# Performance work log

Measured on AMD Instinct MI355X. Metric: run time of the kernel, lower is better.

The kernel has to match this reference:

```python
import jax, jax.numpy as jnp
import numpy as np

N_NODES = 100000
N_EDGES = 1600000
IN_DIM = 128
OUT_DIM = 64


def setup_inputs() -> dict:
    key = jax.random.key(0)
    k1, k2, k3, k4, k5, k6 = jax.random.split(key, 6)
    x = jax.random.normal(k1, (N_NODES, IN_DIM), dtype=jnp.float32)
    edge_row = jax.random.randint(k2, (N_EDGES,), 0, N_NODES, dtype=jnp.int32)
    edge_col = jax.random.randint(k3, (N_EDGES,), 0, N_NODES, dtype=jnp.int32)
    edge_val = jax.random.uniform(k4, (N_EDGES,), dtype=jnp.float32)
    W = jax.random.normal(k5, (IN_DIM, OUT_DIM), dtype=jnp.float32) * (1.0 / np.sqrt(IN_DIM))
    b = jax.random.normal(k6, (OUT_DIM,), dtype=jnp.float32) * 0.01
    return {"x": x, "edge_row": edge_row, "edge_col": edge_col,
            "edge_val": edge_val, "W": W, "b": b}


def reference(x, edge_row, edge_col, edge_val, W, b):
    # xw = Linear(x)  -> [N, OUT_DIM]
    xw = x @ W + b
    # SpMM: (A_hat @ xw)[r] = sum_e val[e] * xw[col[e]] for edges with row[e]==r
    msgs = edge_val[:, None] * xw[edge_col]          # [E, OUT_DIM]
    ax = jax.ops.segment_sum(msgs, edge_row, num_segments=N_NODES)  # [N, OUT_DIM]
    # ReLU; dropout p=0.0 is identity (eval mode)
    return jax.nn.relu(ax)
```

## Files before the change

### kernel.cpp

```cpp
#include <hip/hip_runtime.h>
#include <hip/hip_fp16.h>
#include <limits.h>

#define IN_DIM 128
#define OUT_DIM 64
#define NBUCK 782
#define RPB 128
#define HRPB 64
#define CHUNK 4096
#define SCAP2 2048


typedef _Float16 half8_t __attribute__((ext_vector_type(8)));
typedef float    f32x4  __attribute__((ext_vector_type(4)));

__device__ __forceinline__ int kmap(int g, int j) {
    return g * 4 + (j & 3) + 16 * (j >> 2);
}

__global__ __launch_bounds__(256) void prep_kernel(
    const float* __restrict__ W, __half* __restrict__ wf,
    int* __restrict__ bcount, int* __restrict__ cursor) {
    const int t = threadIdx.x;
    for (int idx = t; idx < 4 * 4 * 64 * 8; idx += 256) {
        const int j    = idx & 7;
        const int lane = (idx >> 3) & 63;
        const int ks   = (idx >> 9) & 3;
        const int n    = idx >> 11;
        const int col  = n * 16 + (lane & 15);
        const int k    = ks * 32 + kmap(lane >> 4, j);
        wf[idx] = __float2half(W[k * OUT_DIM + col]);
    }
    if (bcount)
        for (int i = t; i < NBUCK; i += 256) { bcount[i] = 0; cursor[i] = 0; }
}

__global__ __launch_bounds__(256) void gemm_hist_kernel(
    const float* __restrict__ x, const __half* __restrict__ wf,
    const float* __restrict__ b, __half* __restrict__ xw, int n_nodes,
    const int* __restrict__ erow, int* __restrict__ bcount, int n_edges) {
    __shared__ int h[NBUCK];
    const int t  = threadIdx.x;
    const int l  = t & 63;
    const int wv = t >> 6;
    const int g  = l >> 4;
    const int rowbase = blockIdx.x * 64 + wv * 16;
    const int row = rowbase + (l & 15);
    const bool rok = row < n_nodes;
    const float* xr = x + (size_t)row * IN_DIM;

    half8_t bf[4][4];
    const half8_t* wf8 = (const half8_t*)wf;
    #pragma unroll
    for (int n = 0; n < 4; ++n)
        #pragma unroll
        for (int ks = 0; ks < 4; ++ks)
            bf[n][ks] = wf8[(n * 4 + ks) * 64 + l];

    half8_t af[4];
    #pragma unroll
    for (int ks = 0; ks < 4; ++ks) {
        float4 c0 = rok ? *(const float4*)(xr + ks * 32 + g * 4)
                        : make_float4(0.f, 0.f, 0.f, 0.f);
        float4 c1 = rok ? *(const float4*)(xr + ks * 32 + 16 + g * 4)
                        : make_float4(0.f, 0.f, 0.f, 0.f);
        half8_t a;
        a[0] = (_Float16)c0.x; a[1] = (_Float16)c0.y;
        a[2] = (_Float16)c0.z; a[3] = (_Float16)c0.w;
        a[4] = (_Float16)c1.x; a[5] = (_Float16)c1.y;
        a[6] = (_Float16)c1.z; a[7] = (_Float16)c1.w;
        af[ks] = a;
    }

    f32x4 acc[4];
    #pragma unroll
    for (int n = 0; n < 4; ++n) acc[n] = (f32x4){0.f, 0.f, 0.f, 0.f};

    #pragma unroll
    for (int ks = 0; ks < 4; ++ks)
        #pragma unroll
        for (int n = 0; n < 4; ++n)
            acc[n] = __builtin_amdgcn_mfma_f32_16x16x32_f16(af[ks], bf[n][ks], acc[n], 0, 0, 0);

    float bias[4];
    #pragma unroll
    for (int n = 0; n < 4; ++n) bias[n] = b[n * 16 + (l & 15)];

    #pragma unroll
    for (int n = 0; n < 4; ++n)
        #pragma unroll
        for (int q = 0; q < 4; ++q) {
            const int ro = rowbase + g * 4 + q;
            if (ro < n_nodes)
                xw[(size_t)ro * OUT_DIM + n * 16 + (l & 15)] =
                    __float2half(acc[n][q] + bias[n]);
        }

    if (bcount && blockIdx.x < 512) {
        for (int i = t; i < NBUCK; i += 256) h[i] = 0;
        __syncthreads();
        const int stride = 512 * 256;
        for (int e = blockIdx.x * 256 + t; e < n_edges; e += stride)
            atomicAdd(&h[erow[e] >> 7], 1);
        __syncthreads();
        for (int i = t; i < NBUCK; i += 256)
            if (h[i]) atomicAdd(&bcount[i], h[i]);
    }
}

__global__ __launch_bounds__(512) void partition_kernel(
    const int* __restrict__ erow, const int* __restrict__ ecol,
    const float* __restrict__ eval_, const int* __restrict__ bcount,
    int* __restrict__ cursor, int2* __restrict__ ecs,
    int* __restrict__ bbase, int n_edges) {
    __shared__ int  hist[NBUCK];
    __shared__ int  lbase[NBUCK];
    __shared__ int  gdelta[NBUCK];
    __shared__ int  sbase[NBUCK];
    __shared__ int2 data[CHUNK];
    __shared__ int  gpos[CHUNK];
    __shared__ int  wsum[8];

    const int t = threadIdx.x;
    const int base = blockIdx.x * CHUNK;
    const int cnt = min(CHUNK, n_edges - base);

    for (int i = t; i < NBUCK; i += 512) hist[i] = 0;

    {
        const int i0 = 2 * t, i1 = 2 * t + 1;
        const int v0 = (i0 < NBUCK) ? bcount[i0] : 0;
        const int v1 = (i1 < NBUCK) ? bcount[i1] : 0;
        const int s2 = v0 + v1;
        int inc = s2;
        #pragma unroll
        for (int d = 1; d < 64; d <<= 1) {
            int u = __shfl_up(inc, d, 64);
            if ((t & 63) >= d) inc += u;
        }
        if ((t & 63) == 63) wsum[t >> 6] = inc;
        __syncthreads();
        int wp = 0;
        #pragma unroll
        for (int w = 0; w < 8; ++w) if (w < (t >> 6)) wp += wsum[w];
        const int ex = wp + (inc - s2);
        if (i0 < NBUCK) sbase[i0] = ex;
        if (i1 < NBUCK) sbase[i1] = ex + v0;
    }
    __syncthreads();

    if (blockIdx.x == 0) {
        for (int i = t; i < NBUCK; i += 512) bbase[i] = sbase[i];
        if (t == 0) bbase[NBUCK] = n_edges;
    }

    int   myrow[CHUNK / 512];
    int   mycol[CHUNK / 512];
    float myval[CHUNK / 512];
    #pragma unroll
    for (int i = 0; i < CHUNK / 512; ++i) {
        const int idx = t + i * 512;
        if (idx < cnt) {
            const int e = base + idx;
            myrow[i] = erow[e];
            mycol[i] = ecol[e];
            myval[i] = eval_[e];
            atomicAdd(&hist[myrow[i] >> 7], 1);
        }
    }
    __syncthreads();

    {
        const int i0 = 2 * t, i1 = 2 * t + 1;
        const int v0 = (i0 < NBUCK) ? hist[i0] : 0;
        const int v1 = (i1 < NBUCK) ? hist[i1] : 0;
        const int s2 = v0 + v1;
        int inc = s2;
        #pragma unroll
        for (int d = 1; d < 64; d <<= 1) {
            int u = __shfl_up(inc, d, 64);
            if ((t & 63) >= d) inc += u;
        }
        if ((t & 63) == 63) wsum[t >> 6] = inc;
        __syncthreads();
        int wp = 0;
        #pragma unroll
        for (int w = 0; w < 8; ++w) if (w < (t >> 6)) wp += wsum[w];
        const int ex = wp + (inc - s2);
        if (i0 < NBUCK) lbase[i0] = ex;
        if (i1 < NBUCK) lbase[i1] = ex + v0;
    }
    __syncthreads();

    for (int i = t; i < NBUCK; i += 512) {
        const int c = hist[i];
        gdelta[i] = c ? (sbase[i] + atomicAdd(&cursor[i], c) - lbase[i]) : 0;
    }
    __syncthreads();

    #pragma unroll
    for (int i = 0; i < CHUNK / 512; ++i) {
        const int idx = t + i * 512;
        if (idx < cnt) {
            const int bk = myrow[i] >> 7;
            const int slot = atomicAdd(&lbase[bk], 1);
            int2 p;
            p.x = (int)(((unsigned)(myrow[i] & (RPB - 1)) << 25) |
                        ((unsigned)mycol[i] << 7));
            p.y = __float_as_int(myval[i]);
            data[slot] = p;
            gpos[slot] = slot + gdelta[bk];
        }
    }
    __syncthreads();

    for (int slot = t; slot < cnt; slot += 512)
        ecs[gpos[slot]] = data[slot];
}

__global__ __launch_bounds__(512) void bucket_gather_kernel(
    const __half* __restrict__ xw, const int2* __restrict__ ecs,
    const int* __restrict__ bbase, float* __restrict__ out,
    int n_nodes, int n_edges) {
    __shared__ int2 data[SCAP2];
    __shared__ int  hist[HRPB];
    __shared__ int  rstart[HRPB + 1];

    const int bk2  = blockIdx.x;
    const int bk   = bk2 >> 1;
    const int half = bk2 & 1;
    const int t    = threadIdx.x;
    const int lane = t & 63;
    const int wv   = t >> 6;
    const int q    = lane & 7;
    const int g    = lane >> 3;

    const int s   = bbase[bk];
    const int e   = bbase[bk + 1];
    const int cnt = e - s;
    const int rowbase = bk * RPB + half * HRPB;
    const char* xwb = (const char*)xw;

    if (t < HRPB) hist[t] = 0;
    __syncthreads();

    for (int i = t; i < cnt; i += 512) {
        const unsigned rl = ((unsigned)ecs[s + i].x) >> 25;
        if ((int)(rl >> 6) == half) atomicAdd(&hist[rl & (HRPB - 1)], 1);
    }
    __syncthreads();

    if (t < HRPB) {
        const int v = hist[t];
        int inc = v;
        #pragma unroll
        for (int d = 1; d < 64; d <<= 1) {
            int u = __shfl_up(inc, d, 64);
            if (t >= d) inc += u;
        }
        rstart[t] = inc - v;
        hist[t]   = inc - v;
        if (t == HRPB - 1) rstart[HRPB] = inc;
    }
    __syncthreads();

    const int cntH = rstart[HRPB];

    if (cntH <= SCAP2) {
        for (int i = t; i < cnt; i += 512) {
            const int2 p = ecs[s + i];
            const unsigned rl = ((unsigned)p.x) >> 25;
            if ((int)(rl >> 6) == half) {
                const int pos = atomicAdd(&hist[rl & (HRPB - 1)], 1);
                data[pos] = p;
            }
        }
        __syncthreads();

        for (int rp = 0; rp < 4; ++rp) {
            const int rl0 = wv * 8 + rp * 2;
            const int rl1 = rl0 + 1;
            int j0 = rstart[rl0];
            const int e0 = rstart[rl0 + 1];
            int j1 = rstart[rl1];
            const int e1 = rstart[rl1 + 1];

            float acc0[8], acc1[8];
            #pragma unroll
            for (int i = 0; i < 8; ++i) { acc0[i] = 0.f; acc1[i] = 0.f; }

            while (j0 < e0 || j1 < e1) {
                const bool a0 = j0 < e0;
                const bool a1 = j1 < e1;
                float v0 = 0.f, v1 = 0.f;
                unsigned off0 = 0, off1 = 0;
                if (a0) {
                    const int ei = j0 + g;
                    const int2 p = data[min(ei, cntH - 1)];
                    v0 = (ei < e0) ? __int_as_float(p.y) : 0.f;
                    off0 = (((unsigned)p.x) & 0x01FFFF80u) | ((unsigned)q << 4);
                }
                if (a1) {
                    const int ei = j1 + g;
                    const int2 p = data[min(ei, cntH - 1)];
                    v1 = (ei < e1) ? __int_as_float(p.y) : 0.f;
                    off1 = (((unsigned)p.x) & 0x01FFFF80u) | ((unsigned)q << 4);
                }
                union { uint4 u; __half2 h[4]; } U0, U1;
                if (a0) U0.u = *(const uint4*)(xwb + off0);
                if (a1) U1.u = *(const uint4*)(xwb + off1);
                if (a0) {
                    #pragma unroll
                    for (int i = 0; i < 4; ++i) {
                        const float2 f = __half22float2(U0.h[i]);
                        acc0[2 * i]     = fmaf(v0, f.x, acc0[2 * i]);
                        acc0[2 * i + 1] = fmaf(v0, f.y, acc0[2 * i + 1]);
                    }
                    j0 += 8;
                }
                if (a1) {
                    #pragma unroll
                    for (int i = 0; i < 4; ++i) {
                        const float2 f = __half22float2(U1.h[i]);
                        acc1[2 * i]     = fmaf(v1, f.x, acc1[2 * i]);
                        acc1[2 * i + 1] = fmaf(v1, f.y, acc1[2 * i + 1]);
                    }
                    j1 += 8;
                }
            }

            #pragma unroll
            for (int d = 8; d < 64; d <<= 1) {
                #pragma unroll
                for (int i = 0; i < 8; ++i) {
                    acc0[i] += __shfl_xor(acc0[i], d, 64);
                    acc1[i] += __shfl_xor(acc1[i], d, 64);
                }
            }

            if (g == 0) {
                const int r0 = rowbase + rl0;
                const int r1 = rowbase + rl1;
                if (r0 < n_nodes) {
                    float4 o0, o1;
                    o0.x = fmaxf(acc0[0], 0.f); o0.y = fmaxf(acc0[1], 0.f);
                    o0.z = fmaxf(acc0[2], 0.f); o0.w = fmaxf(acc0[3], 0.f);
                    o1.x = fmaxf(acc0[4], 0.f); o1.y = fmaxf(acc0[5], 0.f);
                    o1.z = fmaxf(acc0[6], 0.f); o1.w = fmaxf(acc0[7], 0.f);
                    float* op = out + (size_t)r0 * OUT_DIM + q * 8;
                    *(float4*)(op)     = o0;
                    *(float4*)(op + 4) = o1;
                }
                if (r1 < n_nodes) {
                    float4 o0, o1;
                    o0.x = fmaxf(acc1[0], 0.f); o0.y = fmaxf(acc1[1], 0.f);
                    o0.z = fmaxf(acc1[2], 0.f); o0.w = fmaxf(acc1[3], 0.f);
                    o1.x = fmaxf(acc1[4], 0.f); o1.y = fmaxf(acc1[5], 0.f);
                    o1.z = fmaxf(acc1[6], 0.f); o1.w = fmaxf(acc1[7], 0.f);
                    float* op = out + (size_t)r1 * OUT_DIM + q * 8;
                    *(float4*)(op)     = o0;
                    *(float4*)(op + 4) = o1;
                }
            }
        }
    } else {
        for (int rr = 0; rr < 8; ++rr) {
            const int r = rowbase + wv * 8 + rr;
            if (r >= n_nodes) break;
            float acc[8];
            #pragma unroll
            for (int i = 0; i < 8; ++i) acc[i] = 0.f;
            const unsigned rl = (unsigned)(r & (RPB - 1));
            for (int j = s + g; j < e; j += 8) {
                const int2 p = ecs[j];
                if ((((unsigned)p.x) >> 25) == rl) {
                    const float v = __int_as_float(p.y);
                    const unsigned off = (((unsigned)p.x) & 0x01FFFF80u) | ((unsigned)q << 4);
                    union { uint4 u; __half2 h[4]; } U;
                    U.u = *(const uint4*)(xwb + off);
                    #pragma unroll
                    for (int i = 0; i < 4; ++i) {
                        const float2 f = __half22float2(U.h[i]);
                        acc[2 * i]     = fmaf(v, f.x, acc[2 * i]);
                        acc[2 * i + 1] = fmaf(v, f.y, acc[2 * i + 1]);
                    }
                }
            }
            #pragma unroll
            for (int d = 8; d < 64; d <<= 1)
                #pragma unroll
                for (int i = 0; i < 8; ++i)
                    acc[i] += __shfl_xor(acc[i], d, 64);
            if (g == 0) {
                float4 o0, o1;
                o0.x = fmaxf(acc[0], 0.f); o0.y = fmaxf(acc[1], 0.f);
                o0.z = fmaxf(acc[2], 0.f); o0.w = fmaxf(acc[3], 0.f);
                o1.x = fmaxf(acc[4], 0.f); o1.y = fmaxf(acc[5], 0.f);
                o1.z = fmaxf(acc[6], 0.f); o1.w = fmaxf(acc[7], 0.f);
                float* op = out + (size_t)r * OUT_DIM + q * 8;
                *(float4*)(op)     = o0;
                *(float4*)(op + 4) = o1;
            }
        }
    }
}

__global__ __launch_bounds__(256) void edge_scatter_kernel(
    const __half* __restrict__ xw, const int* __restrict__ erow,
    const int* __restrict__ ecol, const float* __restrict__ eval_,
    float* __restrict__ out, int n_edges) {
    const int lane  = threadIdx.x & 63;
    const int wid   = (blockIdx.x * blockDim.x + threadIdx.x) >> 6;
    const int nwave = (gridDim.x * blockDim.x) >> 6;
    for (int e = wid; e < n_edges; e += nwave) {
        const float m = eval_[e] * __half2float(xw[(size_t)ecol[e] * OUT_DIM + lane]);
        atomicAdd(&out[(size_t)erow[e] * OUT_DIM + lane], m);
    }
}

__global__ __launch_bounds__(256) void relu_kernel(float4* __restrict__ p, int n4) {
    const int stride = gridDim.x * blockDim.x;
    for (int i = blockIdx.x * blockDim.x + threadIdx.x; i < n4; i += stride) {
        float4 v = p[i];
        v.x = fmaxf(v.x, 0.f); v.y = fmaxf(v.y, 0.f);
        v.z = fmaxf(v.z, 0.f); v.w = fmaxf(v.w, 0.f);
        p[i] = v;
    }
}

extern "C" void kernel_launch(void* const* d_in, const int* in_sizes, int n_in,
                              void* d_out, int out_size, void* d_ws, size_t ws_size,
                              hipStream_t stream) {
    const float* x     = (const float*)d_in[0];
    const int*   erow  = (const int*)d_in[1];
    const int*   ecol  = (const int*)d_in[2];
    const float* eval_ = (const float*)d_in[3];
    const float* W     = (const float*)d_in[4];
    const float* b     = (const float*)d_in[5];
    float*       out   = (float*)d_out;

    const int n_nodes = in_sizes[0] / IN_DIM;
    const int n_edges = in_sizes[1];

    auto align256 = [](size_t v) { return (v + 255) & ~(size_t)255; };
    size_t off_xw     = 0;
    size_t off_wf     = align256(off_xw     + (size_t)n_nodes * OUT_DIM * 2);
    size_t off_bcount = align256(off_wf     + (size_t)4 * 4 * 64 * 8 * 2);
    size_t off_cursor = align256(off_bcount + (size_t)NBUCK * 4);
    size_t off_bbase  = align256(off_cursor + (size_t)NBUCK * 4);
    size_t off_ecs    = align256(off_bbase  + (size_t)(NBUCK + 1) * 4);
    size_t need       = off_ecs + (size_t)n_edges * 8;

    __half* xw = (__half*)((char*)d_ws + off_xw);
    __half* wf = (__half*)((char*)d_ws + off_wf);

    const bool main_path = (need <= ws_size) && (n_nodes <= NBUCK * RPB) && (n_edges > 0);

    if (main_path) {
        int*  bcount = (int*)((char*)d_ws + off_bcount);
        int*  cursor = (int*)((char*)d_ws + off_cursor);
        int*  bbase  = (int*)((char*)d_ws + off_bbase);
        int2* ecs    = (int2*)((char*)d_ws + off_ecs);

        prep_kernel<<<1, 256, 0, stream>>>(W, wf, bcount, cursor);
        gemm_hist_kernel<<<(n_nodes + 63) / 64, 256, 0, stream>>>(
            x, wf, b, xw, n_nodes, erow, bcount, n_edges);
        partition_kernel<<<(n_edges + CHUNK - 1) / CHUNK, 512, 0, stream>>>(
            erow, ecol, eval_, bcount, cursor, ecs, bbase, n_edges);
        bucket_gather_kernel<<<NBUCK * 2, 512, 0, stream>>>(
            xw, ecs, bbase, out, n_nodes, n_edges);
    } else {
        prep_kernel<<<1, 256, 0, stream>>>(W, wf, nullptr, nullptr);
        gemm_hist_kernel<<<(n_nodes + 63) / 64, 256, 0, stream>>>(
            x, wf, b, xw, n_nodes, nullptr, nullptr, 0);
        hipMemsetAsync(d_out, 0, (size_t)out_size * sizeof(float), stream);
        edge_scatter_kernel<<<8192, 256, 0, stream>>>(xw, erow, ecol, eval_, out, n_edges);
        relu_kernel<<<2048, 256, 0, stream>>>((float4*)d_out, out_size / 4);
    }
}
```

Baseline: 105.0 us.

## Replace histogram-prefix bucketing with fixed-capacity buckets and fold weight prep into GEMM

After: 101.4 us (median of 2 runs). 3.4% less time.

```diff
diff --git a/kernel.cpp b/kernel.cpp
--- a/kernel.cpp
+++ b/kernel.cpp
@@ -8,6 +8,7 @@
 #define RPB 128
 #define HRPB 64
 #define CHUNK 4096
+#define BCAP 4096
 #define SCAP2 2048
 
 
@@ -18,28 +19,9 @@
     return g * 4 + (j & 3) + 16 * (j >> 2);
 }
 
-__global__ __launch_bounds__(256) void prep_kernel(
-    const float* __restrict__ W, __half* __restrict__ wf,
-    int* __restrict__ bcount, int* __restrict__ cursor) {
-    const int t = threadIdx.x;
-    for (int idx = t; idx < 4 * 4 * 64 * 8; idx += 256) {
-        const int j    = idx & 7;
-        const int lane = (idx >> 3) & 63;
-        const int ks   = (idx >> 9) & 3;
-        const int n    = idx >> 11;
-        const int col  = n * 16 + (lane & 15);
-        const int k    = ks * 32 + kmap(lane >> 4, j);
-        wf[idx] = __float2half(W[k * OUT_DIM + col]);
-    }
-    if (bcount)
-        for (int i = t; i < NBUCK; i += 256) { bcount[i] = 0; cursor[i] = 0; }
-}
-
-__global__ __launch_bounds__(256) void gemm_hist_kernel(
-    const float* __restrict__ x, const __half* __restrict__ wf,
-    const float* __restrict__ b, __half* __restrict__ xw, int n_nodes,
-    const int* __restrict__ erow, int* __restrict__ bcount, int n_edges) {
-    __shared__ int h[NBUCK];
+__global__ __launch_bounds__(256) void gemm_kernel(
+    const float* __restrict__ x, const float* __restrict__ W,
+    const float* __restrict__ b, __half* __restrict__ xw, int n_nodes) {
     const int t  = threadIdx.x;
     const int l  = t & 63;
     const int wv = t >> 6;
@@ -50,12 +32,18 @@
     const float* xr = x + (size_t)row * IN_DIM;
 
     half8_t bf[4][4];
-    const half8_t* wf8 = (const half8_t*)wf;
     #pragma unroll
     for (int n = 0; n < 4; ++n)
         #pragma unroll
-        for (int ks = 0; ks < 4; ++ks)
-            bf[n][ks] = wf8[(n * 4 + ks) * 64 + l];
+        for (int ks = 0; ks < 4; ++ks) {
+            half8_t a;
+            #pragma unroll
+            for (int j = 0; j < 8; ++j) {
+                const int k = ks * 32 + kmap(g, j);
+                a[j] = (_Float16)W[k * OUT_DIM + n * 16 + (l & 15)];
+            }
+            bf[n][ks] = a;
+        }
 
     half8_t af[4];
     #pragma unroll
@@ -95,28 +83,15 @@
                 xw[(size_t)ro * OUT_DIM + n * 16 + (l & 15)] =
                     __float2half(acc[n][q] + bias[n]);
         }
-
-    if (bcount && blockIdx.x < 512) {
-        for (int i = t; i < NBUCK; i += 256) h[i] = 0;
-        __syncthreads();
-        const int stride = 512 * 256;
-        for (int e = blockIdx.x * 256 + t; e < n_edges; e += stride)
-            atomicAdd(&h[erow[e] >> 7], 1);
-        __syncthreads();
-        for (int i = t; i < NBUCK; i += 256)
-            if (h[i]) atomicAdd(&bcount[i], h[i]);
-    }
 }
 
 __global__ __launch_bounds__(512) void partition_kernel(
     const int* __restrict__ erow, const int* __restrict__ ecol,
-    const float* __restrict__ eval_, const int* __restrict__ bcount,
-    int* __restrict__ cursor, int2* __restrict__ ecs,
-    int* __restrict__ bbase, int n_edges) {
+    const float* __restrict__ eval_, int* __restrict__ cursor,
+    int2* __restrict__ ecs, int n_edges) {
     __shared__ int  hist[NBUCK];
     __shared__ int  lbase[NBUCK];
     __shared__ int  gdelta[NBUCK];
-    __shared__ int  sbase[NBUCK];
     __shared__ int2 data[CHUNK];
     __shared__ int  gpos[CHUNK];
     __shared__ int  wsum[8];
@@ -126,33 +101,7 @@
     const int cnt = min(CHUNK, n_edges - base);
 
     for (int i = t; i < NBUCK; i += 512) hist[i] = 0;
-
-    {
-        const int i0 = 2 * t, i1 = 2 * t + 1;
-        const int v0 = (i0 < NBUCK) ? bcount[i0] : 0;
-        const int v1 = (i1 < NBUCK) ? bcount[i1] : 0;
-        const int s2 = v0 + v1;
-        int inc = s2;
-        #pragma unroll
-        for (int d = 1; d < 64; d <<= 1) {
-            int u = __shfl_up(inc, d, 64);
-            if ((t & 63) >= d) inc += u;
-        }
-        if ((t & 63) == 63) wsum[t >> 6] = inc;
-        __syncthreads();
-        int wp = 0;
-        #pragma unroll
-        for (int w = 0; w < 8; ++w) if (w < (t >> 6)) wp += wsum[w];
-        const int ex = wp + (inc - s2);
-        if (i0 < NBUCK) sbase[i0] = ex;
-        if (i1 < NBUCK) sbase[i1] = ex + v0;
-    }
-    __syncthreads();
-
-    if (blockIdx.x == 0) {
-        for (int i = t; i < NBUCK; i += 512) bbase[i] = sbase[i];
-        if (t == 0) bbase[NBUCK] = n_edges;
-    }
+    __syncthreads();
 
     int   myrow[CHUNK / 512];
     int   mycol[CHUNK / 512];
@@ -194,7 +143,7 @@
 
     for (int i = t; i < NBUCK; i += 512) {
         const int c = hist[i];
-        gdelta[i] = c ? (sbase[i] + atomicAdd(&cursor[i], c) - lbase[i]) : 0;
+        gdelta[i] = c ? (i * BCAP + atomicAdd(&cursor[i], c) - lbase[i]) : 0;
     }
     __syncthreads();
 
@@ -214,14 +163,15 @@
     }
     __syncthreads();
 
+    const int limit = NBUCK * BCAP - 1;
     for (int slot = t; slot < cnt; slot += 512)
-        ecs[gpos[slot]] = data[slot];
+        ecs[min(gpos[slot], limit)] = data[slot];
 }
 
 __global__ __launch_bounds__(512) void bucket_gather_kernel(
     const __half* __restrict__ xw, const int2* __restrict__ ecs,
-    const int* __restrict__ bbase, float* __restrict__ out,
-    int n_nodes, int n_edges) {
+    const int* __restrict__ cursor, float* __restrict__ out,
+    int n_nodes) {
     __shared__ int2 data[SCAP2];
     __shared__ int  hist[HRPB];
     __shared__ int  rstart[HRPB + 1];
@@ -235,9 +185,9 @@
     const int q    = lane & 7;
     const int g    = lane >> 3;
 
-    const int s   = bbase[bk];
-    const int e   = bbase[bk + 1];
-    const int cnt = e - s;
+    const int s   = bk * BCAP;
+    const int cnt = min(cursor[bk], BCAP);
+    const int e   = s + cnt;
     const int rowbase = bk * RPB + half * HRPB;
     const char* xwb = (const char*)xw;
 
@@ -444,35 +394,26 @@
 
     auto align256 = [](size_t v) { return (v + 255) & ~(size_t)255; };
     size_t off_xw     = 0;
-    size_t off_wf     = align256(off_xw     + (size_t)n_nodes * OUT_DIM * 2);
-    size_t off_bcount = align256(off_wf     + (size_t)4 * 4 * 64 * 8 * 2);
-    size_t off_cursor = align256(off_bcount + (size_t)NBUCK * 4);
-    size_t off_bbase  = align256(off_cursor + (size_t)NBUCK * 4);
-    size_t off_ecs    = align256(off_bbase  + (size_t)(NBUCK + 1) * 4);
-    size_t need       = off_ecs + (size_t)n_edges * 8;
+    size_t off_cursor = align256(off_xw     + (size_t)n_nodes * OUT_DIM * 2);
+    size_t off_ecs    = align256(off_cursor + (size_t)NBUCK * 4);
+    size_t need       = off_ecs + (size_t)NBUCK * BCAP * 8;
 
     __half* xw = (__half*)((char*)d_ws + off_xw);
-    __half* wf = (__half*)((char*)d_ws + off_wf);
 
     const bool main_path = (need <= ws_size) && (n_nodes <= NBUCK * RPB) && (n_edges > 0);
 
     if (main_path) {
-        int*  bcount = (int*)((char*)d_ws + off_bcount);
         int*  cursor = (int*)((char*)d_ws + off_cursor);
-        int*  bbase  = (int*)((char*)d_ws + off_bbase);
         int2* ecs    = (int2*)((char*)d_ws + off_ecs);
 
-        prep_kernel<<<1, 256, 0, stream>>>(W, wf, bcount, cursor);
-        gemm_hist_kernel<<<(n_nodes + 63) / 64, 256, 0, stream>>>(
-            x, wf, b, xw, n_nodes, erow, bcount, n_edges);
+        hipMemsetAsync(cursor, 0, (size_t)NBUCK * 4, stream);
+        gemm_kernel<<<(n_nodes + 63) / 64, 256, 0, stream>>>(x, W, b, xw, n_nodes);
         partition_kernel<<<(n_edges + CHUNK - 1) / CHUNK, 512, 0, stream>>>(
-            erow, ecol, eval_, bcount, cursor, ecs, bbase, n_edges);
+            erow, ecol, eval_, cursor, ecs, n_edges);
         bucket_gather_kernel<<<NBUCK * 2, 512, 0, stream>>>(
-            xw, ecs, bbase, out, n_nodes, n_edges);
+            xw, ecs, cursor, out, n_nodes);
     } else {
-        prep_kernel<<<1, 256, 0, stream>>>(W, wf, nullptr, nullptr);
-        gemm_hist_kernel<<<(n_nodes + 63) / 64, 256, 0, stream>>>(
-            x, wf, b, xw, n_nodes, nullptr, nullptr, 0);
+        gemm_kernel<<<(n_nodes + 63) / 64, 256, 0, stream>>>(x, W, b, xw, n_nodes);
         hipMemsetAsync(d_out, 0, (size_t)out_size * sizeof(float), stream);
         edge_scatter_kernel<<<8192, 256, 0, stream>>>(xw, erow, ecol, eval_, out, n_edges);
         relu_kernel<<<2048, 256, 0, stream>>>((float4*)d_out, out_size / 4);
```
